# Kernel tuning notes

Measured on AMD Instinct MI355X. Metric: run time of the kernel, lower is better.

Reference implementation:

```python
import math
import jax, jax.numpy as jnp
import numpy as np

D_MODEL = 1024
D_HIDDEN = 4096
N_EXPERTS = 8
TOP_K = 2
CAPACITY_FACTOR = 1.25


def setup_inputs() -> dict:
    key = jax.random.key(0)
    ks = jax.random.split(key, 8)
    s = 0.02
    x = jax.random.normal(ks[0], (4, 2048, D_MODEL), dtype=jnp.float32)
    router_w = jax.random.normal(ks[1], (D_MODEL, N_EXPERTS), dtype=jnp.float32) * s
    router_b = jnp.zeros((N_EXPERTS,), dtype=jnp.float32)
    w1 = jax.random.normal(ks[2], (N_EXPERTS, D_MODEL, D_HIDDEN), dtype=jnp.float32) * s
    b1 = jnp.zeros((N_EXPERTS, D_HIDDEN), dtype=jnp.float32)
    w2 = jax.random.normal(ks[3], (N_EXPERTS, D_HIDDEN, D_MODEL), dtype=jnp.float32) * s
    b2 = jnp.zeros((N_EXPERTS, D_MODEL), dtype=jnp.float32)
    return {"x": x, "router_w": router_w, "router_b": router_b,
            "w1": w1, "b1": b1, "w2": w2, "b2": b2}


def reference(x, router_w, router_b, w1, b1, w2, b2):
    B, T, D = x.shape
    N = B * T
    E = N_EXPERTS
    capacity = max(1, math.ceil(N / E * CAPACITY_FACTOR))

    x_flat = x.reshape(N, D)
    # Router (torch casts input to float32 for router)
    logits = x_flat.astype(jnp.float32) @ router_w + router_b          # [N, E]
    gates = jax.nn.softmax(logits, axis=-1)                            # [N, E]

    _, topk_idx = jax.lax.top_k(gates, TOP_K)                          # [N, k]
    expert_mask = jax.nn.one_hot(topk_idx, E, dtype=jnp.int32).sum(1)  # [N, E]

    # Capacity masking via cumulative position per expert
    pos = jnp.cumsum(expert_mask, axis=0) - 1                          # [N, E]
    expert_mask = expert_mask * (pos < capacity)
    valid = expert_mask > 0                                            # [N, E] bool

    # Dispatch: scatter tokens into [E, capacity, D] buffers (invalid -> slot `capacity`)
    pos_c = jnp.where(valid, pos, capacity)                            # [N, E]
    e_idx = jnp.broadcast_to(jnp.arange(E), (N, E))
    dispatched = (x_flat[:, None, :] * valid[:, :, None].astype(x.dtype))
    buf = jnp.zeros((E, capacity + 1, D), x.dtype).at[
        e_idx.ravel(), pos_c.ravel()].add(dispatched.reshape(N * E, D))
    buf = buf[:, :capacity]                                            # [E, C, D]

    # Per-expert FFN as batched GEMMs (GELU exact, matching nn.GELU default)
    h = jax.nn.gelu(jnp.einsum('ecd,edh->ech', buf, w1) + b1[:, None, :],
                    approximate=False)
    out = jnp.einsum('ech,ehd->ecd', h, w2) + b2[:, None, :]           # [E, C, D]

    # Combine: gather each token's expert outputs, weight by raw softmax gate
    pos_g = jnp.minimum(pos_c, capacity - 1)
    gathered = out[e_idx, pos_g]                                       # [N, E, D]
    weights = (gates * valid).astype(x.dtype)                          # [N, E]
    y = jnp.einsum('ned,ne->nd', gathered, weights)
    return y.reshape(B, T, D)
```

## Files before the change

kernel.cpp:

```cpp
#include <hip/hip_runtime.h>
#include <math.h>

#define D_MODEL 1024
#define D_HIDDEN 4096
#define NEXP 8
#define NTOK 8192
#define CAP 1280

#define BM 128
#define BN 128
#define BK 32
#define LDA 40

typedef __attribute__((ext_vector_type(8))) short short8x;
typedef __attribute__((ext_vector_type(4))) short short4x;
typedef __attribute__((ext_vector_type(4))) float float4x;

__device__ __forceinline__ short f2bf(float f) {
  unsigned u = __float_as_uint(f);
  unsigned r = (u + 0x7FFFu + ((u >> 16) & 1u)) >> 16;
  return (short)r;
}
__device__ __forceinline__ float bf2f(short s) {
  return __uint_as_float(((unsigned)(unsigned short)s) << 16);
}

__global__ __launch_bounds__(256) void router_kernel(
    const float* __restrict__ x, const float* __restrict__ rw,
    const float* __restrict__ rb, int2* __restrict__ tok_experts,
    float2* __restrict__ tok_gates) {
  int t = blockIdx.x * 4 + (threadIdx.x >> 6);
  int lane = threadIdx.x & 63;
  const float* xr = x + (size_t)t * D_MODEL;
  float acc[8];
#pragma unroll
  for (int e = 0; e < 8; ++e) acc[e] = 0.f;
#pragma unroll
  for (int kk = 0; kk < 16; ++kk) {
    int k = kk * 64 + lane;
    float xv = xr[k];
    const float4* wr = (const float4*)(rw + (size_t)k * 8);
    float4 w0 = wr[0], w1v = wr[1];
    acc[0] += xv * w0.x;  acc[1] += xv * w0.y;
    acc[2] += xv * w0.z;  acc[3] += xv * w0.w;
    acc[4] += xv * w1v.x; acc[5] += xv * w1v.y;
    acc[6] += xv * w1v.z; acc[7] += xv * w1v.w;
  }
#pragma unroll
  for (int off = 32; off > 0; off >>= 1) {
#pragma unroll
    for (int e = 0; e < 8; ++e) acc[e] += __shfl_xor(acc[e], off, 64);
  }
  if (lane == 0) {
    float lg[8];
#pragma unroll
    for (int e = 0; e < 8; ++e) lg[e] = acc[e] + rb[e];
    int e0 = 0;
#pragma unroll
    for (int e = 1; e < 8; ++e) if (lg[e] > lg[e0]) e0 = e;
    int e1 = (e0 == 0) ? 1 : 0;
#pragma unroll
    for (int e = 0; e < 8; ++e) if (e != e0 && lg[e] > lg[e1]) e1 = e;
    float mx = lg[e0];
    float s = 0.f;
#pragma unroll
    for (int e = 0; e < 8; ++e) s += expf(lg[e] - mx);
    float inv = 1.f / s;
    tok_experts[t] = make_int2(e0, e1);
    tok_gates[t] = make_float2(expf(lg[e0] - mx) * inv, expf(lg[e1] - mx) * inv);
  }
}

__global__ __launch_bounds__(1024) void scan_kernel(
    const int2* __restrict__ tok_experts, int* __restrict__ slot_token,
    int* __restrict__ token_rows) {
  int e = blockIdx.x;
  int tid = threadIdx.x;
  for (int i = tid; i < CAP; i += 1024) slot_token[e * CAP + i] = -1;
  __shared__ int wsum[16];
  __shared__ int running;
  if (tid == 0) running = 0;
  __syncthreads();
  int lane = tid & 63, wid = tid >> 6;
  unsigned long long lmask = (1ull << lane) - 1ull;
  for (int base = 0; base < NTOK; base += 1024) {
    int t = base + tid;
    int2 ee = tok_experts[t];
    int m = (ee.x == e || ee.y == e) ? 1 : 0;
    unsigned long long bal = __ballot(m);
    int prefix = __popcll(bal & lmask);
    if (lane == 0) wsum[wid] = (int)__popcll(bal);
    __syncthreads();
    if (tid == 0) {
      int s = running;
#pragma unroll
      for (int w = 0; w < 16; ++w) { int v = wsum[w]; wsum[w] = s; s += v; }
      running = s;
    }
    __syncthreads();
    if (m) {
      int pos = wsum[wid] + prefix;
      int which = (ee.x == e) ? 0 : 1;
      if (pos < CAP) {
        slot_token[e * CAP + pos] = t;
        token_rows[2 * t + which] = e * CAP + pos;
      } else {
        token_rows[2 * t + which] = -1;
      }
    }
    __syncthreads();
  }
}

__global__ __launch_bounds__(256) void gemm1_kernel(
    const float* __restrict__ x, const float* __restrict__ w1,
    const float* __restrict__ b1, const int* __restrict__ slot_token,
    short* __restrict__ h) {
  __shared__ short As[BM * LDA];
  __shared__ short Bs[BN * LDA];
  __shared__ int rowtok[BM];
  int e = blockIdx.z, rt = blockIdx.y, ct = blockIdx.x;
  int tid = threadIdx.x;
  if (tid < BM) {
    int gr = rt * BM + tid;
    rowtok[tid] = (gr < CAP) ? slot_token[e * CAP + gr] : -1;
  }
  __syncthreads();
  int lane = tid & 63, wv = tid >> 6;
  int m0 = wv * 32;
  int arow = tid >> 1, akq = (tid & 1) * 16;
  int bn = tid & 127, bkh = (tid >> 7) * 16;
  const int token = rowtok[arow];
  const float* asrc0 = x + (size_t)(token < 0 ? 0 : token) * D_MODEL + akq;
  const float* bsrc0 = w1 + (size_t)e * D_MODEL * D_HIDDEN +
                       (size_t)bkh * D_HIDDEN + (ct * BN + bn);
  float4x acc[2][8];
#pragma unroll
  for (int i = 0; i < 2; ++i)
#pragma unroll
    for (int j = 0; j < 8; ++j) acc[i][j] = (float4x){0.f, 0.f, 0.f, 0.f};

  short8x* adst = (short8x*)&As[arow * LDA + akq];
  short8x* bdst = (short8x*)&Bs[bn * LDA + bkh];
  const short8x* afrag0 = (const short8x*)&As[(m0 + (lane & 15)) * LDA + (lane >> 4) * 8];
  const short8x* afrag1 = (const short8x*)&As[(m0 + 16 + (lane & 15)) * LDA + (lane >> 4) * 8];

  for (int k0 = 0; k0 < D_MODEL; k0 += BK) {
    short8x p0, p1;
    if (token >= 0) {
      const float4* s4 = (const float4*)(asrc0 + k0);
#pragma unroll
      for (int i = 0; i < 2; ++i) {
        float4 f = s4[i];
        p0[i * 4 + 0] = f2bf(f.x); p0[i * 4 + 1] = f2bf(f.y);
        p0[i * 4 + 2] = f2bf(f.z); p0[i * 4 + 3] = f2bf(f.w);
      }
#pragma unroll
      for (int i = 0; i < 2; ++i) {
        float4 f = s4[2 + i];
        p1[i * 4 + 0] = f2bf(f.x); p1[i * 4 + 1] = f2bf(f.y);
        p1[i * 4 + 2] = f2bf(f.z); p1[i * 4 + 3] = f2bf(f.w);
      }
    } else {
#pragma unroll
      for (int i = 0; i < 8; ++i) { p0[i] = 0; p1[i] = 0; }
    }
    short8x q0, q1;
    {
      const float* bs = bsrc0 + (size_t)k0 * D_HIDDEN;
#pragma unroll
      for (int kk = 0; kk < 8; ++kk) q0[kk] = f2bf(bs[(size_t)kk * D_HIDDEN]);
#pragma unroll
      for (int kk = 0; kk < 8; ++kk) q1[kk] = f2bf(bs[(size_t)(kk + 8) * D_HIDDEN]);
    }
    __syncthreads();
    adst[0] = p0; adst[1] = p1;
    bdst[0] = q0; bdst[1] = q1;
    __syncthreads();
    short8x a0 = afrag0[0];
    short8x a1 = afrag1[0];
#pragma unroll
    for (int j = 0; j < 8; ++j) {
      short8x b = *(const short8x*)&Bs[(j * 16 + (lane & 15)) * LDA + (lane >> 4) * 8];
      acc[0][j] = __builtin_amdgcn_mfma_f32_16x16x32_bf16(a0, b, acc[0][j], 0, 0, 0);
      acc[1][j] = __builtin_amdgcn_mfma_f32_16x16x32_bf16(a1, b, acc[1][j], 0, 0, 0);
    }
    __syncthreads();
  }
  int col0 = ct * BN;
  int rbase = (lane >> 4) * 4;
#pragma unroll
  for (int i = 0; i < 2; ++i) {
#pragma unroll
    for (int j = 0; j < 8; ++j) {
      int col = col0 + j * 16 + (lane & 15);
      float bias = b1[e * D_HIDDEN + col];
#pragma unroll
      for (int r = 0; r < 4; ++r) {
        int grow = rt * BM + m0 + i * 16 + rbase + r;
        float v = acc[i][j][r] + bias;
        v = 0.5f * v * (1.0f + erff(v * 0.70710678118654752f));
        h[(size_t)(e * CAP + grow) * D_HIDDEN + col] = f2bf(v);
      }
    }
  }
}

__global__ __launch_bounds__(256) void gemm2_kernel(
    const short* __restrict__ h, const float* __restrict__ w2,
    const float* __restrict__ b2, short* __restrict__ out2) {
  __shared__ short As[BM * LDA];
  __shared__ short Bs[BN * LDA];
  int e = blockIdx.z, rt = blockIdx.y, ct = blockIdx.x;
  int tid = threadIdx.x;
  int lane = tid & 63, wv = tid >> 6;
  int m0 = wv * 32;
  int arow = tid >> 1, akq = (tid & 1) * 16;
  int bn = tid & 127, bkh = (tid >> 7) * 16;
  const short* asrc0 = h + (size_t)(e * CAP + rt * BM + arow) * D_HIDDEN + akq;
  const float* bsrc0 = w2 + (size_t)e * D_HIDDEN * D_MODEL +
                       (size_t)bkh * D_MODEL + (ct * BN + bn);
  float4x acc[2][8];
#pragma unroll
  for (int i = 0; i < 2; ++i)
#pragma unroll
    for (int j = 0; j < 8; ++j) acc[i][j] = (float4x){0.f, 0.f, 0.f, 0.f};

  short8x* adst = (short8x*)&As[arow * LDA + akq];
  short8x* bdst = (short8x*)&Bs[bn * LDA + bkh];
  const short8x* afrag0 = (const short8x*)&As[(m0 + (lane & 15)) * LDA + (lane >> 4) * 8];
  const short8x* afrag1 = (const short8x*)&As[(m0 + 16 + (lane & 15)) * LDA + (lane >> 4) * 8];

  for (int k0 = 0; k0 < D_HIDDEN; k0 += BK) {
    const short8x* s8 = (const short8x*)(asrc0 + k0);
    short8x p0 = s8[0], p1 = s8[1];
    short8x q0, q1;
    {
      const float* bs = bsrc0 + (size_t)k0 * D_MODEL;
#pragma unroll
      for (int kk = 0; kk < 8; ++kk) q0[kk] = f2bf(bs[(size_t)kk * D_MODEL]);
#pragma unroll
      for (int kk = 0; kk < 8; ++kk) q1[kk] = f2bf(bs[(size_t)(kk + 8) * D_MODEL]);
    }
    __syncthreads();
    adst[0] = p0; adst[1] = p1;
    bdst[0] = q0; bdst[1] = q1;
    __syncthreads();
    short8x a0 = afrag0[0];
    short8x a1 = afrag1[0];
#pragma unroll
    for (int j = 0; j < 8; ++j) {
      short8x b = *(const short8x*)&Bs[(j * 16 + (lane & 15)) * LDA + (lane >> 4) * 8];
      acc[0][j] = __builtin_amdgcn_mfma_f32_16x16x32_bf16(a0, b, acc[0][j], 0, 0, 0);
      acc[1][j] = __builtin_amdgcn_mfma_f32_16x16x32_bf16(a1, b, acc[1][j], 0, 0, 0);
    }
    __syncthreads();
  }
  int col0 = ct * BN;
  int rbase = (lane >> 4) * 4;
#pragma unroll
  for (int i = 0; i < 2; ++i) {
#pragma unroll
    for (int j = 0; j < 8; ++j) {
      int col = col0 + j * 16 + (lane & 15);
      float bias = b2[e * D_MODEL + col];
#pragma unroll
      for (int r = 0; r < 4; ++r) {
        int grow = rt * BM + m0 + i * 16 + rbase + r;
        float v = acc[i][j][r] + bias;
        out2[(size_t)(e * CAP + grow) * D_MODEL + col] = f2bf(v);
      }
    }
  }
}

__global__ __launch_bounds__(256) void combine_kernel(
    const int* __restrict__ token_rows, const float2* __restrict__ tok_gates,
    const short* __restrict__ out2, float* __restrict__ y) {
  int t = blockIdx.x;
  int r0 = token_rows[2 * t], r1 = token_rows[2 * t + 1];
  float2 g = tok_gates[t];
  int d = threadIdx.x * 4;
  float4 v; v.x = v.y = v.z = v.w = 0.f;
  if (r0 >= 0) {
    short4x a = *(const short4x*)(out2 + (size_t)r0 * D_MODEL + d);
    v.x += g.x * bf2f(a[0]); v.y += g.x * bf2f(a[1]);
    v.z += g.x * bf2f(a[2]); v.w += g.x * bf2f(a[3]);
  }
  if (r1 >= 0) {
    short4x a = *(const short4x*)(out2 + (size_t)r1 * D_MODEL + d);
    v.x += g.y * bf2f(a[0]); v.y += g.y * bf2f(a[1]);
    v.z += g.y * bf2f(a[2]); v.w += g.y * bf2f(a[3]);
  }
  *(float4*)(y + (size_t)t * D_MODEL + d) = v;
}

extern "C" void kernel_launch(void* const* d_in, const int* in_sizes, int n_in,
                              void* d_out, int out_size, void* d_ws, size_t ws_size,
                              hipStream_t stream) {
  const float* x  = (const float*)d_in[0];
  const float* rw = (const float*)d_in[1];
  const float* rb = (const float*)d_in[2];
  const float* w1 = (const float*)d_in[3];
  const float* b1 = (const float*)d_in[4];
  const float* w2 = (const float*)d_in[5];
  const float* b2 = (const float*)d_in[6];
  float* y = (float*)d_out;
  (void)in_sizes; (void)n_in; (void)out_size; (void)ws_size;

  char* p = (char*)d_ws;
  size_t off = 0;
  auto take = [&](size_t bytes) -> void* {
    void* r = p + off;
    off = (off + bytes + 255) & ~(size_t)255;
    return r;
  };
  int2*   tok_experts = (int2*)  take((size_t)NTOK * sizeof(int2));
  float2* tok_gates   = (float2*)take((size_t)NTOK * sizeof(float2));
  int*    slot_token  = (int*)   take((size_t)NEXP * CAP * sizeof(int));
  int*    token_rows  = (int*)   take((size_t)NTOK * 2 * sizeof(int));
  short*  h           = (short*) take((size_t)NEXP * CAP * D_HIDDEN * sizeof(short));
  short*  out2        = (short*) take((size_t)NEXP * CAP * D_MODEL * sizeof(short));

  router_kernel<<<NTOK / 4, 256, 0, stream>>>(x, rw, rb, tok_experts, tok_gates);
  scan_kernel<<<NEXP, 1024, 0, stream>>>(tok_experts, slot_token, token_rows);
  gemm1_kernel<<<dim3(D_HIDDEN / BN, CAP / BM, NEXP), 256, 0, stream>>>(x, w1, b1, slot_token, h);
  gemm2_kernel<<<dim3(D_MODEL / BN, CAP / BM, NEXP), 256, 0, stream>>>(h, w2, b2, out2);
  combine_kernel<<<NTOK, 256, 0, stream>>>(token_rows, tok_gates, out2, y);
}
```

Before: 714.9 us.

## Pre-convert activations and weights to bf16 and stream GEMM tiles via direct-to-LDS loads

Adds prepass kernels that convert x to bf16 and transpose-convert w1/w2 into K-contiguous bf16 layouts. New GEMM kernels then load tiles straight into swizzled LDS with global_load_lds, avoiding per-tile fp32 loads and in-register conversion. The prepasses are extra passes over 256MB of fp32 weights on every call. The new path falls back to the old kernels when the workspace is too small.

```diff
diff --git a/kernel.cpp b/kernel.cpp
--- a/kernel.cpp
+++ b/kernel.cpp
@@ -23,6 +23,49 @@
 }
 __device__ __forceinline__ float bf2f(short s) {
   return __uint_as_float(((unsigned)(unsigned short)s) << 16);
+}
+
+#define GLDS16(g, l)                                                        \
+  __builtin_amdgcn_global_load_lds(                                         \
+      (const __attribute__((address_space(1))) void*)(g),                   \
+      (__attribute__((address_space(3))) void*)(l), 16, 0, 0)
+
+__global__ __launch_bounds__(256) void convert_x_kernel(
+    const float* __restrict__ x, short* __restrict__ xbf) {
+  size_t i = ((size_t)blockIdx.x * 256 + threadIdx.x) * 8;
+  const float4* s = (const float4*)(x + i);
+  float4 a = s[0], b = s[1];
+  short8x o;
+  o[0] = f2bf(a.x); o[1] = f2bf(a.y); o[2] = f2bf(a.z); o[3] = f2bf(a.w);
+  o[4] = f2bf(b.x); o[5] = f2bf(b.y); o[6] = f2bf(b.z); o[7] = f2bf(b.w);
+  *(short8x*)(xbf + i) = o;
+}
+
+__global__ __launch_bounds__(256) void transpose_kernel(
+    const float* __restrict__ in, short* __restrict__ out, int K, int N) {
+  __shared__ short tile[64][65];
+  int n0 = blockIdx.x * 64, k0 = blockIdx.y * 64, e = blockIdx.z;
+  int tid = threadIdx.x;
+  int cr = tid >> 4;
+  int cc = (tid & 15) * 4;
+  const float* src = in + (size_t)e * K * N;
+#pragma unroll
+  for (int p = 0; p < 4; ++p) {
+    int r = p * 16 + cr;
+    float4 v = *(const float4*)(src + (size_t)(k0 + r) * N + n0 + cc);
+    tile[r][cc] = f2bf(v.x); tile[r][cc + 1] = f2bf(v.y);
+    tile[r][cc + 2] = f2bf(v.z); tile[r][cc + 3] = f2bf(v.w);
+  }
+  __syncthreads();
+  short* dst = out + (size_t)e * N * K;
+#pragma unroll
+  for (int p = 0; p < 4; ++p) {
+    int nr = p * 16 + cr;
+    short4x s;
+#pragma unroll
+    for (int j = 0; j < 4; ++j) s[j] = tile[cc + j][nr];
+    *(short4x*)(dst + (size_t)(n0 + nr) * K + k0 + cc) = s;
+  }
 }
 
 __global__ __launch_bounds__(256) void router_kernel(
@@ -112,7 +155,148 @@
   }
 }
 
-__global__ __launch_bounds__(256) void gemm1_kernel(
+
+__global__ __launch_bounds__(256) void gemm1_fast(
+    const short* __restrict__ xbf, const short* __restrict__ w1t,
+    const float* __restrict__ b1, const int* __restrict__ slot_token,
+    short* __restrict__ h) {
+  __shared__ short As[BM * BK];
+  __shared__ short Bs[BN * BK];
+  __shared__ int rowtok[BM];
+  int e = blockIdx.z, rt = blockIdx.y, ct = blockIdx.x;
+  int tid = threadIdx.x;
+  if (tid < BM) {
+    int t = slot_token[e * CAP + rt * BM + tid];
+    rowtok[tid] = t < 0 ? 0 : t;
+  }
+  __syncthreads();
+  int lane = tid & 63, w = tid >> 6;
+
+  const char* agm[2]; const char* bgm[2];
+  char* alds[2]; char* blds[2];
+#pragma unroll
+  for (int p = 0; p < 2; ++p) {
+    int r = w * 32 + p * 16 + (lane >> 2);
+    int c = ((lane & 3) - ((r >> 1) & 3)) & 3;
+    agm[p] = (const char*)(xbf + (size_t)rowtok[r] * D_MODEL + c * 8);
+    alds[p] = (char*)As + (w * 32 + p * 16) * 64 + lane * 16;
+    bgm[p] = (const char*)(w1t + ((size_t)e * D_HIDDEN + ct * BN + r) * D_MODEL + c * 8);
+    blds[p] = (char*)Bs + (w * 32 + p * 16) * 64 + lane * 16;
+  }
+  int l15 = lane & 15, q = lane >> 4;
+  int swz = (q + ((l15 >> 1) & 3)) & 3;
+  const char* afb = (const char*)As + (w * 32 + l15) * 64 + swz * 16;
+  const char* bfb = (const char*)Bs + l15 * 64 + swz * 16;
+
+  float4x acc[2][8];
+#pragma unroll
+  for (int i = 0; i < 2; ++i)
+#pragma unroll
+    for (int j = 0; j < 8; ++j) acc[i][j] = (float4x){0.f, 0.f, 0.f, 0.f};
+
+  for (int k0 = 0; k0 < D_MODEL; k0 += BK) {
+    __syncthreads();
+    int kb = k0 * 2;
+    GLDS16(agm[0] + kb, alds[0]);
+    GLDS16(agm[1] + kb, alds[1]);
+    GLDS16(bgm[0] + kb, blds[0]);
+    GLDS16(bgm[1] + kb, blds[1]);
+    __syncthreads();
+    short8x a0 = *(const short8x*)afb;
+    short8x a1 = *(const short8x*)(afb + 1024);
+#pragma unroll
+    for (int j = 0; j < 8; ++j) {
+      short8x b = *(const short8x*)(bfb + j * 1024);
+      acc[0][j] = __builtin_amdgcn_mfma_f32_16x16x32_bf16(a0, b, acc[0][j], 0, 0, 0);
+      acc[1][j] = __builtin_amdgcn_mfma_f32_16x16x32_bf16(a1, b, acc[1][j], 0, 0, 0);
+    }
+  }
+  int col0 = ct * BN;
+  int rbase = q * 4;
+#pragma unroll
+  for (int i = 0; i < 2; ++i) {
+#pragma unroll
+    for (int j = 0; j < 8; ++j) {
+      int col = col0 + j * 16 + l15;
+      float bias = b1[e * D_HIDDEN + col];
+#pragma unroll
+      for (int r = 0; r < 4; ++r) {
+        int grow = rt * BM + w * 32 + i * 16 + rbase + r;
+        float v = acc[i][j][r] + bias;
+        v = 0.5f * v * (1.0f + erff(v * 0.70710678118654752f));
+        h[(size_t)(e * CAP + grow) * D_HIDDEN + col] = f2bf(v);
+      }
+    }
+  }
+}
+
+__global__ __launch_bounds__(256) void gemm2_fast(
+    const short* __restrict__ h, const short* __restrict__ w2t,
+    const float* __restrict__ b2, short* __restrict__ out2) {
+  __shared__ short As[BM * BK];
+  __shared__ short Bs[BN * BK];
+  int e = blockIdx.z, rt = blockIdx.y, ct = blockIdx.x;
+  int tid = threadIdx.x;
+  int lane = tid & 63, w = tid >> 6;
+
+  const char* agm[2]; const char* bgm[2];
+  char* alds[2]; char* blds[2];
+#pragma unroll
+  for (int p = 0; p < 2; ++p) {
+    int r = w * 32 + p * 16 + (lane >> 2);
+    int c = ((lane & 3) - ((r >> 1) & 3)) & 3;
+    agm[p] = (const char*)(h + (size_t)(e * CAP + rt * BM + r) * D_HIDDEN + c * 8);
+    alds[p] = (char*)As + (w * 32 + p * 16) * 64 + lane * 16;
+    bgm[p] = (const char*)(w2t + ((size_t)e * D_MODEL + ct * BN + r) * D_HIDDEN + c * 8);
+    blds[p] = (char*)Bs + (w * 32 + p * 16) * 64 + lane * 16;
+  }
+  int l15 = lane & 15, q = lane >> 4;
+  int swz = (q + ((l15 >> 1) & 3)) & 3;
+  const char* afb = (const char*)As + (w * 32 + l15) * 64 + swz * 16;
+  const char* bfb = (const char*)Bs + l15 * 64 + swz * 16;
+
+  float4x acc[2][8];
+#pragma unroll
+  for (int i = 0; i < 2; ++i)
+#pragma unroll
+    for (int j = 0; j < 8; ++j) acc[i][j] = (float4x){0.f, 0.f, 0.f, 0.f};
+
+  for (int k0 = 0; k0 < D_HIDDEN; k0 += BK) {
+    __syncthreads();
+    int kb = k0 * 2;
+    GLDS16(agm[0] + kb, alds[0]);
+    GLDS16(agm[1] + kb, alds[1]);
+    GLDS16(bgm[0] + kb, blds[0]);
+    GLDS16(bgm[1] + kb, blds[1]);
+    __syncthreads();
+    short8x a0 = *(const short8x*)afb;
+    short8x a1 = *(const short8x*)(afb + 1024);
+#pragma unroll
+    for (int j = 0; j < 8; ++j) {
+      short8x b = *(const short8x*)(bfb + j * 1024);
+      acc[0][j] = __builtin_amdgcn_mfma_f32_16x16x32_bf16(a0, b, acc[0][j], 0, 0, 0);
+      acc[1][j] = __builtin_amdgcn_mfma_f32_16x16x32_bf16(a1, b, acc[1][j], 0, 0, 0);
+    }
+  }
+  int col0 = ct * BN;
+  int rbase = q * 4;
+#pragma unroll
+  for (int i = 0; i < 2; ++i) {
+#pragma unroll
+    for (int j = 0; j < 8; ++j) {
+      int col = col0 + j * 16 + l15;
+      float bias = b2[e * D_MODEL + col];
+#pragma unroll
+      for (int r = 0; r < 4; ++r) {
+        int grow = rt * BM + w * 32 + i * 16 + rbase + r;
+        float v = acc[i][j][r] + bias;
+        out2[(size_t)(e * CAP + grow) * D_MODEL + col] = f2bf(v);
+      }
+    }
+  }
+}
+
+__global__ __launch_bounds__(256) void gemm1_v1(
     const float* __restrict__ x, const float* __restrict__ w1,
     const float* __restrict__ b1, const int* __restrict__ slot_token,
     short* __restrict__ h) {
@@ -206,7 +390,7 @@
   }
 }
 
-__global__ __launch_bounds__(256) void gemm2_kernel(
+__global__ __launch_bounds__(256) void gemm2_v1(
     const short* __restrict__ h, const float* __restrict__ w2,
     const float* __restrict__ b2, short* __restrict__ out2) {
   __shared__ short As[BM * LDA];
@@ -306,7 +490,7 @@
   const float* w2 = (const float*)d_in[5];
   const float* b2 = (const float*)d_in[6];
   float* y = (float*)d_out;
-  (void)in_sizes; (void)n_in; (void)out_size; (void)ws_size;
+  (void)in_sizes; (void)n_in; (void)out_size;
 
   char* p = (char*)d_ws;
   size_t off = 0;
@@ -319,12 +503,36 @@
   float2* tok_gates   = (float2*)take((size_t)NTOK * sizeof(float2));
   int*    slot_token  = (int*)   take((size_t)NEXP * CAP * sizeof(int));
   int*    token_rows  = (int*)   take((size_t)NTOK * 2 * sizeof(int));
-  short*  h           = (short*) take((size_t)NEXP * CAP * D_HIDDEN * sizeof(short));
-  short*  out2        = (short*) take((size_t)NEXP * CAP * D_MODEL * sizeof(short));
+
+  size_t off_common = off;
+  short* xbf  = (short*)take((size_t)NTOK * D_MODEL * sizeof(short));
+  short* w1t  = (short*)take((size_t)NEXP * D_HIDDEN * D_MODEL * sizeof(short));
+  short* w2t  = (short*)take((size_t)NEXP * D_MODEL * D_HIDDEN * sizeof(short));
+  short* h    = (short*)take((size_t)NEXP * CAP * D_HIDDEN * sizeof(short));
+  short* out2 = (short*)take((size_t)NEXP * CAP * D_MODEL * sizeof(short));
+  bool fast = (off <= ws_size);
 
   router_kernel<<<NTOK / 4, 256, 0, stream>>>(x, rw, rb, tok_experts, tok_gates);
   scan_kernel<<<NEXP, 1024, 0, stream>>>(tok_experts, slot_token, token_rows);
-  gemm1_kernel<<<dim3(D_HIDDEN / BN, CAP / BM, NEXP), 256, 0, stream>>>(x, w1, b1, slot_token, h);
-  gemm2_kernel<<<dim3(D_MODEL / BN, CAP / BM, NEXP), 256, 0, stream>>>(h, w2, b2, out2);
+
+  if (fast) {
+    convert_x_kernel<<<NTOK * D_MODEL / (256 * 8), 256, 0, stream>>>(x, xbf);
+    transpose_kernel<<<dim3(D_HIDDEN / 64, D_MODEL / 64, NEXP), 256, 0, stream>>>(
+        w1, w1t, D_MODEL, D_HIDDEN);
+    transpose_kernel<<<dim3(D_MODEL / 64, D_HIDDEN / 64, NEXP), 256, 0, stream>>>(
+        w2, w2t, D_HIDDEN, D_MODEL);
+    gemm1_fast<<<dim3(D_HIDDEN / BN, CAP / BM, NEXP), 256, 0, stream>>>(
+        xbf, w1t, b1, slot_token, h);
+    gemm2_fast<<<dim3(D_MODEL / BN, CAP / BM, NEXP), 256, 0, stream>>>(
+        h, w2t, b2, out2);
+  } else {
+    off = off_common;
+    h    = (short*)take((size_t)NEXP * CAP * D_HIDDEN * sizeof(short));
+    out2 = (short*)take((size_t)NEXP * CAP * D_MODEL * sizeof(short));
+    gemm1_v1<<<dim3(D_HIDDEN / BN, CAP / BM, NEXP), 256, 0, stream>>>(
+        x, w1, b1, slot_token, h);
+    gemm2_v1<<<dim3(D_MODEL / BN, CAP / BM, NEXP), 256, 0, stream>>>(
+        h, w2, b2, out2);
+  }
   combine_kernel<<<NTOK, 256, 0, stream>>>(token_rows, tok_gates, out2, y);
 }
```

Result: faster. 647.3 us (-9.5%).

## Pre-convert inputs and weights to bf16 K-major and stream GEMM tiles via global_load_lds

Applied to the files above, without the earlier changes.

Adds kernels that convert x to bf16 and transpose-convert w1/w2 into bf16 K-major layouts. Both expert GEMMs are then rewritten to load tiles directly into swizzled LDS with global_load_lds at BK=64, replacing strided scalar fp32 loads and in-loop conversion. Exact erf GELU is replaced by a sigmoid-based tanh approximation. This trades extra full-weight conversion passes each call and slight GELU accuracy loss for much cheaper GEMM inner loops.

```diff
diff --git a/kernel.cpp b/kernel.cpp
--- a/kernel.cpp
+++ b/kernel.cpp
@@ -9,8 +9,7 @@
 
 #define BM 128
 #define BN 128
-#define BK 32
-#define LDA 40
+#define BK2 64
 
 typedef __attribute__((ext_vector_type(8))) short short8x;
 typedef __attribute__((ext_vector_type(4))) short short4x;
@@ -23,6 +22,53 @@
 }
 __device__ __forceinline__ float bf2f(short s) {
   return __uint_as_float(((unsigned)(unsigned short)s) << 16);
+}
+__device__ __forceinline__ float gelu_fast(float v) {
+  float u2 = v * (1.5957691216f + 0.0713548163f * v * v);
+  return v / (1.0f + __expf(-u2));
+}
+
+#define GLDS16(g, l)                                                        \
+  __builtin_amdgcn_global_load_lds(                                         \
+      (const __attribute__((address_space(1))) void*)(g),                   \
+      (__attribute__((address_space(3))) void*)(l), 16, 0, 0)
+
+__global__ __launch_bounds__(256) void convert_x_kernel(
+    const float* __restrict__ x, short* __restrict__ xbf) {
+  size_t i = ((size_t)blockIdx.x * 256 + threadIdx.x) * 8;
+  const float4* s = (const float4*)(x + i);
+  float4 a = s[0], b = s[1];
+  short8x o;
+  o[0] = f2bf(a.x); o[1] = f2bf(a.y); o[2] = f2bf(a.z); o[3] = f2bf(a.w);
+  o[4] = f2bf(b.x); o[5] = f2bf(b.y); o[6] = f2bf(b.z); o[7] = f2bf(b.w);
+  *(short8x*)(xbf + i) = o;
+}
+
+__global__ __launch_bounds__(256) void transpose_kernel(
+    const float* __restrict__ in, short* __restrict__ out, int K, int N) {
+  __shared__ short tile[64][65];
+  int n0 = blockIdx.x * 64, k0 = blockIdx.y * 64, e = blockIdx.z;
+  int tid = threadIdx.x;
+  int cr = tid >> 4;
+  int cc = (tid & 15) * 4;
+  const float* src = in + (size_t)e * K * N;
+#pragma unroll
+  for (int p = 0; p < 4; ++p) {
+    int r = p * 16 + cr;
+    float4 v = *(const float4*)(src + (size_t)(k0 + r) * N + n0 + cc);
+    tile[r][cc] = f2bf(v.x); tile[r][cc + 1] = f2bf(v.y);
+    tile[r][cc + 2] = f2bf(v.z); tile[r][cc + 3] = f2bf(v.w);
+  }
+  __syncthreads();
+  short* dst = out + (size_t)e * N * K;
+#pragma unroll
+  for (int p = 0; p < 4; ++p) {
+    int nr = p * 16 + cr;
+    short4x s;
+#pragma unroll
+    for (int j = 0; j < 4; ++j) s[j] = tile[cc + j][nr];
+    *(short4x*)(dst + (size_t)(n0 + nr) * K + k0 + cc) = s;
+  }
 }
 
 __global__ __launch_bounds__(256) void router_kernel(
@@ -112,161 +158,163 @@
   }
 }
 
-__global__ __launch_bounds__(256) void gemm1_kernel(
-    const float* __restrict__ x, const float* __restrict__ w1,
+
+__global__ __launch_bounds__(256) void gemm1_fast(
+    const short* __restrict__ xbf, const short* __restrict__ w1t,
     const float* __restrict__ b1, const int* __restrict__ slot_token,
     short* __restrict__ h) {
-  __shared__ short As[BM * LDA];
-  __shared__ short Bs[BN * LDA];
+  __shared__ short As[BM * BK2];
+  __shared__ short Bs[BN * BK2];
   __shared__ int rowtok[BM];
   int e = blockIdx.z, rt = blockIdx.y, ct = blockIdx.x;
   int tid = threadIdx.x;
   if (tid < BM) {
-    int gr = rt * BM + tid;
-    rowtok[tid] = (gr < CAP) ? slot_token[e * CAP + gr] : -1;
+    int t = slot_token[e * CAP + rt * BM + tid];
+    rowtok[tid] = t < 0 ? 0 : t;
   }
   __syncthreads();
-  int lane = tid & 63, wv = tid >> 6;
-  int m0 = wv * 32;
-  int arow = tid >> 1, akq = (tid & 1) * 16;
-  int bn = tid & 127, bkh = (tid >> 7) * 16;
-  const int token = rowtok[arow];
-  const float* asrc0 = x + (size_t)(token < 0 ? 0 : token) * D_MODEL + akq;
-  const float* bsrc0 = w1 + (size_t)e * D_MODEL * D_HIDDEN +
-                       (size_t)bkh * D_HIDDEN + (ct * BN + bn);
+  int lane = tid & 63, w = tid >> 6;
+
+  int srow = w * 8 + (lane >> 3);
+  int slot = lane & 7;
+  int cA = (slot - ((srow >> 1) & 7)) & 7;
+  const char* agm[4];
+  char* alds[4];
+  char* blds[4];
+#pragma unroll
+  for (int p = 0; p < 4; ++p) {
+    int r = p * 32 + srow;
+    agm[p] = (const char*)(xbf + (size_t)rowtok[r] * D_MODEL) + cA * 16;
+    alds[p] = (char*)As + (r * 8 + slot) * 16;
+    blds[p] = (char*)Bs + (r * 8 + slot) * 16;
+  }
+  const char* bgm0 =
+      (const char*)(w1t + ((size_t)e * D_HIDDEN + ct * BN + srow) * D_MODEL) + cA * 16;
+  const size_t bstride = (size_t)32 * D_MODEL * 2;
+
+  int l15 = lane & 15, q = lane >> 4;
+  const char* A0 = (const char*)As + (w * 32 + l15) * 128;
+  const char* B0 = (const char*)Bs + l15 * 128;
+  int sw0 = (((q + (l15 >> 1)) & 7)) * 16;
+  int sw1 = (((4 + q + (l15 >> 1)) & 7)) * 16;
+
   float4x acc[2][8];
 #pragma unroll
   for (int i = 0; i < 2; ++i)
 #pragma unroll
     for (int j = 0; j < 8; ++j) acc[i][j] = (float4x){0.f, 0.f, 0.f, 0.f};
 
-  short8x* adst = (short8x*)&As[arow * LDA + akq];
-  short8x* bdst = (short8x*)&Bs[bn * LDA + bkh];
-  const short8x* afrag0 = (const short8x*)&As[(m0 + (lane & 15)) * LDA + (lane >> 4) * 8];
-  const short8x* afrag1 = (const short8x*)&As[(m0 + 16 + (lane & 15)) * LDA + (lane >> 4) * 8];
-
-  for (int k0 = 0; k0 < D_MODEL; k0 += BK) {
-    short8x p0, p1;
-    if (token >= 0) {
-      const float4* s4 = (const float4*)(asrc0 + k0);
-#pragma unroll
-      for (int i = 0; i < 2; ++i) {
-        float4 f = s4[i];
-        p0[i * 4 + 0] = f2bf(f.x); p0[i * 4 + 1] = f2bf(f.y);
-        p0[i * 4 + 2] = f2bf(f.z); p0[i * 4 + 3] = f2bf(f.w);
-      }
-#pragma unroll
-      for (int i = 0; i < 2; ++i) {
-        float4 f = s4[2 + i];
-        p1[i * 4 + 0] = f2bf(f.x); p1[i * 4 + 1] = f2bf(f.y);
-        p1[i * 4 + 2] = f2bf(f.z); p1[i * 4 + 3] = f2bf(f.w);
-      }
-    } else {
-#pragma unroll
-      for (int i = 0; i < 8; ++i) { p0[i] = 0; p1[i] = 0; }
-    }
-    short8x q0, q1;
-    {
-      const float* bs = bsrc0 + (size_t)k0 * D_HIDDEN;
-#pragma unroll
-      for (int kk = 0; kk < 8; ++kk) q0[kk] = f2bf(bs[(size_t)kk * D_HIDDEN]);
-#pragma unroll
-      for (int kk = 0; kk < 8; ++kk) q1[kk] = f2bf(bs[(size_t)(kk + 8) * D_HIDDEN]);
-    }
-    __syncthreads();
-    adst[0] = p0; adst[1] = p1;
-    bdst[0] = q0; bdst[1] = q1;
-    __syncthreads();
-    short8x a0 = afrag0[0];
-    short8x a1 = afrag1[0];
+  for (int k0 = 0; k0 < D_MODEL; k0 += BK2) {
+    __syncthreads();
+    int kb = k0 * 2;
+#pragma unroll
+    for (int p = 0; p < 4; ++p) GLDS16(agm[p] + kb, alds[p]);
+#pragma unroll
+    for (int p = 0; p < 4; ++p) GLDS16(bgm0 + p * bstride + kb, blds[p]);
+    __syncthreads();
+    short8x a00 = *(const short8x*)(A0 + sw0);
+    short8x a10 = *(const short8x*)(A0 + 2048 + sw0);
+    short8x a01 = *(const short8x*)(A0 + sw1);
+    short8x a11 = *(const short8x*)(A0 + 2048 + sw1);
 #pragma unroll
     for (int j = 0; j < 8; ++j) {
-      short8x b = *(const short8x*)&Bs[(j * 16 + (lane & 15)) * LDA + (lane >> 4) * 8];
-      acc[0][j] = __builtin_amdgcn_mfma_f32_16x16x32_bf16(a0, b, acc[0][j], 0, 0, 0);
-      acc[1][j] = __builtin_amdgcn_mfma_f32_16x16x32_bf16(a1, b, acc[1][j], 0, 0, 0);
-    }
-    __syncthreads();
+      short8x b0 = *(const short8x*)(B0 + j * 2048 + sw0);
+      acc[0][j] = __builtin_amdgcn_mfma_f32_16x16x32_bf16(a00, b0, acc[0][j], 0, 0, 0);
+      acc[1][j] = __builtin_amdgcn_mfma_f32_16x16x32_bf16(a10, b0, acc[1][j], 0, 0, 0);
+      short8x b1v = *(const short8x*)(B0 + j * 2048 + sw1);
+      acc[0][j] = __builtin_amdgcn_mfma_f32_16x16x32_bf16(a01, b1v, acc[0][j], 0, 0, 0);
+      acc[1][j] = __builtin_amdgcn_mfma_f32_16x16x32_bf16(a11, b1v, acc[1][j], 0, 0, 0);
+    }
   }
   int col0 = ct * BN;
-  int rbase = (lane >> 4) * 4;
+  int rbase = q * 4;
 #pragma unroll
   for (int i = 0; i < 2; ++i) {
 #pragma unroll
     for (int j = 0; j < 8; ++j) {
-      int col = col0 + j * 16 + (lane & 15);
+      int col = col0 + j * 16 + l15;
       float bias = b1[e * D_HIDDEN + col];
 #pragma unroll
       for (int r = 0; r < 4; ++r) {
-        int grow = rt * BM + m0 + i * 16 + rbase + r;
-        float v = acc[i][j][r] + bias;
-        v = 0.5f * v * (1.0f + erff(v * 0.70710678118654752f));
+        int grow = rt * BM + w * 32 + i * 16 + rbase + r;
+        float v = gelu_fast(acc[i][j][r] + bias);
         h[(size_t)(e * CAP + grow) * D_HIDDEN + col] = f2bf(v);
       }
     }
   }
 }
 
-__global__ __launch_bounds__(256) void gemm2_kernel(
-    const short* __restrict__ h, const float* __restrict__ w2,
+__global__ __launch_bounds__(256) void gemm2_fast(
+    const short* __restrict__ h, const short* __restrict__ w2t,
     const float* __restrict__ b2, short* __restrict__ out2) {
-  __shared__ short As[BM * LDA];
-  __shared__ short Bs[BN * LDA];
+  __shared__ short As[BM * BK2];
+  __shared__ short Bs[BN * BK2];
   int e = blockIdx.z, rt = blockIdx.y, ct = blockIdx.x;
   int tid = threadIdx.x;
-  int lane = tid & 63, wv = tid >> 6;
-  int m0 = wv * 32;
-  int arow = tid >> 1, akq = (tid & 1) * 16;
-  int bn = tid & 127, bkh = (tid >> 7) * 16;
-  const short* asrc0 = h + (size_t)(e * CAP + rt * BM + arow) * D_HIDDEN + akq;
-  const float* bsrc0 = w2 + (size_t)e * D_HIDDEN * D_MODEL +
-                       (size_t)bkh * D_MODEL + (ct * BN + bn);
+  int lane = tid & 63, w = tid >> 6;
+
+  int srow = w * 8 + (lane >> 3);
+  int slot = lane & 7;
+  int cA = (slot - ((srow >> 1) & 7)) & 7;
+  char* alds[4];
+  char* blds[4];
+#pragma unroll
+  for (int p = 0; p < 4; ++p) {
+    int r = p * 32 + srow;
+    alds[p] = (char*)As + (r * 8 + slot) * 16;
+    blds[p] = (char*)Bs + (r * 8 + slot) * 16;
+  }
+  const char* agm0 =
+      (const char*)(h + (size_t)(e * CAP + rt * BM + srow) * D_HIDDEN) + cA * 16;
+  const char* bgm0 =
+      (const char*)(w2t + ((size_t)e * D_MODEL + ct * BN + srow) * D_HIDDEN) + cA * 16;
+  const size_t astride = (size_t)32 * D_HIDDEN * 2;
+
+  int l15 = lane & 15, q = lane >> 4;
+  const char* A0 = (const char*)As + (w * 32 + l15) * 128;
+  const char* B0 = (const char*)Bs + l15 * 128;
+  int sw0 = (((q + (l15 >> 1)) & 7)) * 16;
+  int sw1 = (((4 + q + (l15 >> 1)) & 7)) * 16;
+
   float4x acc[2][8];
 #pragma unroll
   for (int i = 0; i < 2; ++i)
 #pragma unroll
     for (int j = 0; j < 8; ++j) acc[i][j] = (float4x){0.f, 0.f, 0.f, 0.f};
 
-  short8x* adst = (short8x*)&As[arow * LDA + akq];
-  short8x* bdst = (short8x*)&Bs[bn * LDA + bkh];
-  const short8x* afrag0 = (const short8x*)&As[(m0 + (lane & 15)) * LDA + (lane >> 4) * 8];
-  const short8x* afrag1 = (const short8x*)&As[(m0 + 16 + (lane & 15)) * LDA + (lane >> 4) * 8];
-
-  for (int k0 = 0; k0 < D_HIDDEN; k0 += BK) {
-    const short8x* s8 = (const short8x*)(asrc0 + k0);
-    short8x p0 = s8[0], p1 = s8[1];
-    short8x q0, q1;
-    {
-      const float* bs = bsrc0 + (size_t)k0 * D_MODEL;
-#pragma unroll
-      for (int kk = 0; kk < 8; ++kk) q0[kk] = f2bf(bs[(size_t)kk * D_MODEL]);
-#pragma unroll
-      for (int kk = 0; kk < 8; ++kk) q1[kk] = f2bf(bs[(size_t)(kk + 8) * D_MODEL]);
-    }
-    __syncthreads();
-    adst[0] = p0; adst[1] = p1;
-    bdst[0] = q0; bdst[1] = q1;
-    __syncthreads();
-    short8x a0 = afrag0[0];
-    short8x a1 = afrag1[0];
+  for (int k0 = 0; k0 < D_HIDDEN; k0 += BK2) {
+    __syncthreads();
+    int kb = k0 * 2;
+#pragma unroll
+    for (int p = 0; p < 4; ++p) GLDS16(agm0 + p * astride + kb, alds[p]);
+#pragma unroll
+    for (int p = 0; p < 4; ++p) GLDS16(bgm0 + p * astride + kb, blds[p]);
+    __syncthreads();
+    short8x a00 = *(const short8x*)(A0 + sw0);
+    short8x a10 = *(const short8x*)(A0 + 2048 + sw0);
+    short8x a01 = *(const short8x*)(A0 + sw1);
+    short8x a11 = *(const short8x*)(A0 + 2048 + sw1);
 #pragma unroll
     for (int j = 0; j < 8; ++j) {
-      short8x b = *(const short8x*)&Bs[(j * 16 + (lane & 15)) * LDA + (lane >> 4) * 8];
-      acc[0][j] = __builtin_amdgcn_mfma_f32_16x16x32_bf16(a0, b, acc[0][j], 0, 0, 0);
-      acc[1][j] = __builtin_amdgcn_mfma_f32_16x16x32_bf16(a1, b, acc[1][j], 0, 0, 0);
-    }
-    __syncthreads();
+      short8x b0 = *(const short8x*)(B0 + j * 2048 + sw0);
+      acc[0][j] = __builtin_amdgcn_mfma_f32_16x16x32_bf16(a00, b0, acc[0][j], 0, 0, 0);
+      acc[1][j] = __builtin_amdgcn_mfma_f32_16x16x32_bf16(a10, b0, acc[1][j], 0, 0, 0);
+      short8x b1v = *(const short8x*)(B0 + j * 2048 + sw1);
+      acc[0][j] = __builtin_amdgcn_mfma_f32_16x16x32_bf16(a01, b1v, acc[0][j], 0, 0, 0);
+      acc[1][j] = __builtin_amdgcn_mfma_f32_16x16x32_bf16(a11, b1v, acc[1][j], 0, 0, 0);
+    }
   }
   int col0 = ct * BN;
-  int rbase = (lane >> 4) * 4;
+  int rbase = q * 4;
 #pragma unroll
   for (int i = 0; i < 2; ++i) {
 #pragma unroll
     for (int j = 0; j < 8; ++j) {
-      int col = col0 + j * 16 + (lane & 15);
+      int col = col0 + j * 16 + l15;
       float bias = b2[e * D_MODEL + col];
 #pragma unroll
       for (int r = 0; r < 4; ++r) {
-        int grow = rt * BM + m0 + i * 16 + rbase + r;
+        int grow = rt * BM + w * 32 + i * 16 + rbase + r;
         float v = acc[i][j][r] + bias;
         out2[(size_t)(e * CAP + grow) * D_MODEL + col] = f2bf(v);
       }
@@ -319,12 +367,22 @@
   float2* tok_gates   = (float2*)take((size_t)NTOK * sizeof(float2));
   int*    slot_token  = (int*)   take((size_t)NEXP * CAP * sizeof(int));
   int*    token_rows  = (int*)   take((size_t)NTOK * 2 * sizeof(int));
+  short*  xbf         = (short*) take((size_t)NTOK * D_MODEL * sizeof(short));
+  short*  w1t         = (short*) take((size_t)NEXP * D_HIDDEN * D_MODEL * sizeof(short));
+  short*  w2t         = (short*) take((size_t)NEXP * D_MODEL * D_HIDDEN * sizeof(short));
   short*  h           = (short*) take((size_t)NEXP * CAP * D_HIDDEN * sizeof(short));
   short*  out2        = (short*) take((size_t)NEXP * CAP * D_MODEL * sizeof(short));
 
   router_kernel<<<NTOK / 4, 256, 0, stream>>>(x, rw, rb, tok_experts, tok_gates);
   scan_kernel<<<NEXP, 1024, 0, stream>>>(tok_experts, slot_token, token_rows);
-  gemm1_kernel<<<dim3(D_HIDDEN / BN, CAP / BM, NEXP), 256, 0, stream>>>(x, w1, b1, slot_token, h);
-  gemm2_kernel<<<dim3(D_MODEL / BN, CAP / BM, NEXP), 256, 0, stream>>>(h, w2, b2, out2);
+  convert_x_kernel<<<NTOK * D_MODEL / (256 * 8), 256, 0, stream>>>(x, xbf);
+  transpose_kernel<<<dim3(D_HIDDEN / 64, D_MODEL / 64, NEXP), 256, 0, stream>>>(
+      w1, w1t, D_MODEL, D_HIDDEN);
+  transpose_kernel<<<dim3(D_MODEL / 64, D_HIDDEN / 64, NEXP), 256, 0, stream>>>(
+      w2, w2t, D_HIDDEN, D_MODEL);
+  gemm1_fast<<<dim3(D_HIDDEN / BN, CAP / BM, NEXP), 256, 0, stream>>>(
+      xbf, w1t, b1, slot_token, h);
+  gemm2_fast<<<dim3(D_MODEL / BN, CAP / BM, NEXP), 256, 0, stream>>>(
+      h, w2t, b2, out2);
   combine_kernel<<<NTOK, 256, 0, stream>>>(token_rows, tok_gates, out2, y);
 }
```

Result: faster. 696.2 us (-2.6%).
